# Kernel tuning notes

Measured on AMD Instinct MI355X. Metric: run time of the kernel, lower is better.

Reference implementation:

```python
import jax, jax.numpy as jnp
import numpy as np

B, S, D = 2, 2048, 2048
H, KVH, HD = 16, 4, 128
REP = H // KVH  # 4
THETA = 10000.0


def setup_inputs() -> dict:
    key = jax.random.key(0)
    ks = jax.random.split(key, 5)
    scale = 0.02
    x = jax.random.normal(ks[0], (B, S, D), dtype=jnp.float32)
    Wq = jax.random.normal(ks[1], (D, H * HD), dtype=jnp.float32) * scale
    Wk = jax.random.normal(ks[2], (D, KVH * HD), dtype=jnp.float32) * scale
    Wv = jax.random.normal(ks[3], (D, KVH * HD), dtype=jnp.float32) * scale
    Wo = jax.random.normal(ks[4], (H * HD, D), dtype=jnp.float32) * scale
    return {"x": x, "Wq": Wq, "Wk": Wk, "Wv": Wv, "Wo": Wo}


def _rope_cos_sin(seq_len, dtype):
    # HF-style rotary embedding: inv_freq over even dims, duplicated halves
    inv_freq = 1.0 / (THETA ** (jnp.arange(0, HD, 2, dtype=jnp.float32) / HD))
    pos = jnp.arange(seq_len, dtype=jnp.float32)
    ang = pos[:, None] * inv_freq[None, :]          # [S, HD/2]
    emb = jnp.concatenate([ang, ang], axis=-1)       # [S, HD]
    return jnp.cos(emb).astype(dtype), jnp.sin(emb).astype(dtype)


def _rotate_half(t):
    t1, t2 = jnp.split(t, 2, axis=-1)
    return jnp.concatenate([-t2, t1], axis=-1)


def reference(x, Wq, Wk, Wv, Wo):
    bsz, seq_len, _ = x.shape
    q = (x @ Wq).reshape(bsz, seq_len, H, HD).transpose(0, 2, 1, 3)    # [B,H,S,HD]
    k = (x @ Wk).reshape(bsz, seq_len, KVH, HD).transpose(0, 2, 1, 3)  # [B,KVH,S,HD]
    v = (x @ Wv).reshape(bsz, seq_len, KVH, HD).transpose(0, 2, 1, 3)
    cos, sin = _rope_cos_sin(seq_len, q.dtype)       # [S,HD]
    cos = cos[None, None, :, :]
    sin = sin[None, None, :, :]
    q = q * cos + _rotate_half(q) * sin
    k = k * cos + _rotate_half(k) * sin
    # repeat_interleave KV heads to match Q heads
    k = jnp.repeat(k, REP, axis=1)                   # [B,H,S,HD]
    v = jnp.repeat(v, REP, axis=1)
    scores = jnp.einsum('bhqd,bhkd->bhqk', q, k) / jnp.sqrt(jnp.float32(HD)).astype(q.dtype)
    i = jnp.arange(seq_len)
    causal = jnp.where(i[None, :] > i[:, None], jnp.float32(-jnp.inf), 0.0).astype(scores.dtype)
    scores = scores + causal[None, None, :, :]
    probs = jax.nn.softmax(scores.astype(jnp.float32), axis=-1).astype(q.dtype)
    out = jnp.einsum('bhqk,bhkd->bhqd', probs, v)    # [B,H,S,HD]
    out = out.transpose(0, 2, 1, 3).reshape(bsz, seq_len, H * HD)
    return out @ Wo
```

## Files before the change

### kernel.cpp

```cpp
#include <hip/hip_runtime.h>
#include <math.h>

#define B_   2
#define S_   2048
#define D_   2048
#define H_   16
#define KVH_ 4
#define HD_  128
#define REP_ 4

typedef __attribute__((ext_vector_type(8))) short bf16x8;
typedef __attribute__((ext_vector_type(4))) short bf16x4;
typedef __attribute__((ext_vector_type(4))) float f32x4;

#define QSCALE_LOG2E 0.1275266977097153f

__device__ __forceinline__ unsigned short f2bf(float x) {
    union { float f; unsigned u; } v; v.f = x;
    unsigned r = v.u + 0x7FFF + ((v.u >> 16) & 1);
    return (unsigned short)(r >> 16);
}

__device__ __forceinline__ unsigned short f2bf_fast(float x) {
    union { float f; unsigned u; } v; v.f = x;
    return (unsigned short)((v.u + 0x8000) >> 16);
}

__device__ __forceinline__ void gl_lds16(const unsigned short* g, unsigned short* l) {
    __builtin_amdgcn_global_load_lds(
        (const __attribute__((address_space(1))) unsigned int*)g,
        (__attribute__((address_space(3))) unsigned int*)l,
        16, 0, 0);
}

#define PH_BAR() do { asm volatile("" ::: "memory"); \
                      __builtin_amdgcn_s_barrier();  \
                      asm volatile("" ::: "memory"); } while (0)
#define VMW6 asm volatile("s_waitcnt vmcnt(6)" ::: "memory")
#define VMW4 asm volatile("s_waitcnt vmcnt(4)" ::: "memory")
#define VMW0 asm volatile("s_waitcnt vmcnt(0)" ::: "memory")

__global__ void cast_bf16(const float* __restrict__ src,
                          unsigned short* __restrict__ dst, int n4)
{
    int i = blockIdx.x * 256 + threadIdx.x;
    if (i >= n4) return;
    float4 v = *(const float4*)&src[(size_t)i * 4];
    bf16x4 o;
    o[0] = (short)f2bf(v.x); o[1] = (short)f2bf(v.y);
    o[2] = (short)f2bf(v.z); o[3] = (short)f2bf(v.w);
    *(bf16x4*)&dst[(size_t)i * 4] = o;
}

__global__ __launch_bounds__(256) void cast_transpose_all(
    const float* __restrict__ Wq, const float* __restrict__ Wk,
    const float* __restrict__ Wv, const float* __restrict__ Wo,
    unsigned short* __restrict__ Wqt, unsigned short* __restrict__ Wkt,
    unsigned short* __restrict__ Wvt, unsigned short* __restrict__ Wot)
{
    __shared__ float T[32][33];
    const int y = blockIdx.y;
    const float* src; unsigned short* dst; int C, bj;
    if (y < 64)      { src = Wq; dst = Wqt; C = 2048; bj = y; }
    else if (y < 80) { src = Wk; dst = Wkt; C = 512;  bj = y - 64; }
    else if (y < 96) { src = Wv; dst = Wvt; C = 512;  bj = y - 80; }
    else             { src = Wo; dst = Wot; C = 2048; bj = y - 96; }

    const int bi = blockIdx.x;
    const int t  = threadIdx.x;
    const int r  = t >> 3, cq = (t & 7) * 4;

    float4 v = *(const float4*)&src[(size_t)(bi * 32 + r) * C + bj * 32 + cq];
    T[r][cq + 0] = v.x; T[r][cq + 1] = v.y;
    T[r][cq + 2] = v.z; T[r][cq + 3] = v.w;
    __syncthreads();

    bf16x4 o;
    o[0] = (short)f2bf(T[cq + 0][r]);
    o[1] = (short)f2bf(T[cq + 1][r]);
    o[2] = (short)f2bf(T[cq + 2][r]);
    o[3] = (short)f2bf(T[cq + 3][r]);
    *(bf16x4*)&dst[(size_t)(bj * 32 + r) * 2048 + bi * 32 + cq] = o;
}

__global__ __launch_bounds__(512, 2) void qkv_mfma8(
    const unsigned short* __restrict__ Ah,
    const unsigned short* __restrict__ Wqt,
    const unsigned short* __restrict__ Wkt,
    const unsigned short* __restrict__ Wvt,
    unsigned short* __restrict__ Qh, unsigned short* __restrict__ Kh,
    unsigned short* __restrict__ Vt)
{
    __shared__ __align__(16) unsigned short lds[65536];

    const int bid = blockIdx.x;
    const int swz = (bid & 7) * 24 + (bid >> 3);
    const int bm = swz / 12, bn = swz % 12;
    const int m0 = bm * 256, n0 = bn * 256;

    const int tid  = threadIdx.x;
    const int w    = tid >> 6;
    const int lane = tid & 63;
    const int lo16 = lane & 15, quad = lane >> 4;
    const int wm   = w >> 2, wn = w & 3;

    const unsigned short* Bt;
    if (n0 < 2048)      Bt = Wqt + (size_t)n0 * 2048;
    else if (n0 < 2560) Bt = Wkt + (size_t)(n0 - 2048) * 2048;
    else                Bt = Wvt + (size_t)(n0 - 2560) * 2048;
    const unsigned short* Ag   = Ah + (size_t)m0 * 2048;
    const unsigned short* AgH1 = Ag + (size_t)128 * 2048;
    const unsigned short* BtH1 = Bt + (size_t)128 * 2048;

    const int rs   = lane >> 3;
    const int sce  = (((lane & 7) ^ rs) << 3);
    const int grow = w * 8 + rs;

    #define STAGE(gb, k0, lb) do {                                          \
        const unsigned short* _g = (gb) + (size_t)grow * 2048 + (k0) + sce; \
        gl_lds16(_g,                     (lb) + w * 512);                   \
        gl_lds16(_g + (size_t)64 * 2048, (lb) + (8 + w) * 512);             \
    } while (0)

    const int swb = (lo16 & 7) << 4;
    const int ac0 = (quad << 4) ^ swb;
    const int ac1 = (64 | (quad << 4)) ^ swb;
    char* ldsb = (char*)lds;
    const int abase = (wm * 128 + lo16) * 128;
    const int bbase = (wn * 16 + lo16) * 128 + 32768;

    f32x4 acc[8][4];
    #pragma unroll
    for (int mf = 0; mf < 8; ++mf)
        #pragma unroll
        for (int j = 0; j < 4; ++j) acc[mf][j] = (f32x4){0.f, 0.f, 0.f, 0.f};

    bf16x8 a0[4][2], a1[4][2], b0[2][2], b1[2][2];

    #define MM(Aa, Bb, mo, jo)                                               \
        _Pragma("unroll") for (int mf = 0; mf < 4; ++mf)                     \
        _Pragma("unroll") for (int j = 0; j < 2; ++j) {                      \
            acc[(mo)+mf][(jo)+j] = __builtin_amdgcn_mfma_f32_16x16x32_bf16(  \
                Aa[mf][0], Bb[j][0], acc[(mo)+mf][(jo)+j], 0, 0, 0);         \
            acc[(mo)+mf][(jo)+j] = __builtin_amdgcn_mfma_f32_16x16x32_bf16(  \
                Aa[mf][1], Bb[j][1], acc[(mo)+mf][(jo)+j], 0, 0, 0);         \
        }

    STAGE(Bt,   0,  lds + 16384);
    STAGE(BtH1, 0,  lds + 24576);
    STAGE(Ag,   0,  lds + 0);
    STAGE(AgH1, 0,  lds + 8192);
    STAGE(Bt,   64, lds + 32768 + 16384);
    STAGE(BtH1, 64, lds + 32768 + 24576);
    STAGE(Ag,   64, lds + 32768);
    VMW6;
    PH_BAR();

    #define PHASES(p, t)                                                         \
    {   _Pragma("unroll") for (int mf = 0; mf < 4; ++mf) {                       \
            a0[mf][0] = *(const bf16x8*)(ldsb + (p)*65536 + abase + mf*2048 + ac0); \
            a0[mf][1] = *(const bf16x8*)(ldsb + (p)*65536 + abase + mf*2048 + ac1); \
        }                                                                        \
        _Pragma("unroll") for (int j = 0; j < 2; ++j) {                          \
            b0[j][0] = *(const bf16x8*)(ldsb + (p)*65536 + bbase + j*8192 + ac0); \
            b0[j][1] = *(const bf16x8*)(ldsb + (p)*65536 + bbase + j*8192 + ac1); \
        }                                                                        \
        STAGE(AgH1, ((t)+1)*64, lds + ((p)^1)*32768 + 8192);                     \
        PH_BAR(); __builtin_amdgcn_s_setprio(1);                                 \
        MM(a0, b0, 0, 0);                                                        \
        __builtin_amdgcn_s_setprio(0); PH_BAR();                                 \
        _Pragma("unroll") for (int j = 0; j < 2; ++j) {                          \
            b1[j][0] = *(const bf16x8*)(ldsb + (p)*65536 + bbase + (j+2)*8192 + ac0); \
            b1[j][1] = *(const bf16x8*)(ldsb + (p)*65536 + bbase + (j+2)*8192 + ac1); \
        }                                                                        \
        STAGE(Bt, ((t)+2)*64, lds + (p)*32768 + 16384);                          \
        PH_BAR(); __builtin_amdgcn_s_setprio(1);                                 \
        MM(a0, b1, 0, 2);                                                        \
        __builtin_amdgcn_s_setprio(0); PH_BAR();                                 \
        _Pragma("unroll") for (int mf = 0; mf < 4; ++mf) {                       \
            a1[mf][0] = *(const bf16x8*)(ldsb + (p)*65536 + abase + (mf+4)*2048 + ac0); \
            a1[mf][1] = *(const bf16x8*)(ldsb + (p)*65536 + abase + (mf+4)*2048 + ac1); \
        }                                                                        \
        STAGE(BtH1, ((t)+2)*64, lds + (p)*32768 + 24576);                        \
        PH_BAR(); __builtin_amdgcn_s_setprio(1);                                 \
        MM(a1, b0, 4, 0);                                                        \
        __builtin_amdgcn_s_setprio(0); PH_BAR();                                 \
        STAGE(Ag, ((t)+2)*64, lds + (p)*32768);                                  \
        PH_BAR(); __builtin_amdgcn_s_setprio(1);                                 \
        MM(a1, b1, 4, 2);                                                        \
        __builtin_amdgcn_s_setprio(0);                                           \
        VMW6;                                                                    \
        PH_BAR();                                                                \
    }

    for (int it = 0; it < 16; ++it) {
        const int t = 2 * it;
        PHASES(0, t);
        PHASES(1, t + 1);
    }

    VMW0;
    PH_BAR();

    const int bb = m0 >> 11;
    const int s0loc = m0 & 2047;

    if (n0 < 2560) {
        const bool isQ = (n0 < 2048);
        const int h0 = isQ ? (n0 >> 7) : ((n0 - 2048) >> 7);
        const float post = isQ ? QSCALE_LOG2E : 1.0f;
        unsigned short* db[2];
        #pragma unroll
        for (int hp = 0; hp < 2; ++hp)
            db[hp] = isQ
                ? Qh + (((size_t)bb * H_   + h0 + hp) * S_) * HD_
                : Kh + (((size_t)bb * KVH_ + h0 + hp) * S_) * HD_;
        const int d = wn * 16 + lo16;
        const float inv = exp2f(-(float)d * 0.20761871093344086f);
        #pragma unroll
        for (int mf = 0; mf < 8; ++mf) {
            #pragma unroll
            for (int r = 0; r < 4; ++r) {
                int s = s0loc + wm * 128 + mf * 16 + quad * 4 + r;
                float sn, c;
                sincosf((float)s * inv, &sn, &c);
                #pragma unroll
                for (int hp = 0; hp < 2; ++hp) {
                    float lo = acc[mf][2 * hp + 0][r];
                    float hi = acc[mf][2 * hp + 1][r];
                    unsigned short* drow = db[hp] + (size_t)s * HD_;
                    drow[d]      = f2bf((lo * c - hi * sn) * post);
                    drow[d + 64] = f2bf((hi * c + lo * sn) * post);
                }
            }
        }
    } else {
        const int g0 = (n0 - 2560) >> 7;
        unsigned short* Ts = lds;
        const int d = wn * 16 + lo16;
        #pragma unroll
        for (int hp = 0; hp < 2; ++hp) {
            if (hp) PH_BAR();
            #pragma unroll
            for (int mf = 0; mf < 8; ++mf) {
                int ml = wm * 128 + mf * 16 + quad * 4;
                bf16x4 v0, v1;
                #pragma unroll
                for (int r = 0; r < 4; ++r) {
                    v0[r] = (short)f2bf(acc[mf][2 * hp + 0][r]);
                    v1[r] = (short)f2bf(acc[mf][2 * hp + 1][r]);
                }
                *(bf16x4*)&Ts[(size_t)d        * 264 + ml] = v0;
                *(bf16x4*)&Ts[(size_t)(d + 64) * 264 + ml] = v1;
            }
            PH_BAR();
            unsigned short* dstb = Vt + (((size_t)bb * KVH_ + g0 + hp) * HD_) * S_ + s0loc;
            #pragma unroll
            for (int itb = 0; itb < 8; ++itb) {
                int dd = itb * 16 + (tid >> 5);
                int ch = (tid & 31) * 8;
                *(bf16x8*)(dstb + (size_t)dd * S_ + ch) =
                    *(const bf16x8*)&Ts[(size_t)dd * 264 + ch];
            }
        }
    }
    #undef PHASES
    #undef MM
    #undef STAGE
}

__global__ __launch_bounds__(256, 2) void flash_attn_mfma(
    const unsigned short* __restrict__ Qh,
    const unsigned short* __restrict__ Kh,
    const unsigned short* __restrict__ Vt,
    unsigned short* __restrict__ attb)
{
    const int bh   = blockIdx.x;
    const int yy   = blockIdx.y;
    const int qt   = (yy < 8) ? (15 - yy) : (yy - 8);
    const int b    = bh >> 4, h = bh & 15;
    const int g    = h >> 2;
    const int tid  = threadIdx.x;
    const int w    = tid >> 6;
    const int lane = tid & 63;
    const int lo16 = lane & 15;
    const int quad = lane >> 4;

    const unsigned short* Qb = Qh + (((size_t)b * H_   + h) * S_) * HD_;
    const unsigned short* Kb = Kh + (((size_t)b * KVH_ + g) * S_) * HD_;
    const unsigned short* Vb = Vt + (((size_t)b * KVH_ + g) * HD_) * S_;

    __shared__ __align__(16) unsigned short Ks[64][136];
    __shared__ __align__(16) unsigned short Vs[128][72];
    __shared__ __align__(16) unsigned short Ps[4][32][72];

    const int q0 = qt * 128;
    const int qw = q0 + w * 32;

    bf16x8 qf[2][4];
    #pragma unroll
    for (int st = 0; st < 2; ++st)
        #pragma unroll
        for (int kc = 0; kc < 4; ++kc)
            qf[st][kc] = *(const bf16x8*)(Qb + (size_t)(qw + st * 16 + lo16) * HD_
                                             + kc * 32 + quad * 8);

    f32x4 o[2][8];
    #pragma unroll
    for (int st = 0; st < 2; ++st)
        #pragma unroll
        for (int n = 0; n < 8; ++n) o[st][n] = (f32x4){0.f, 0.f, 0.f, 0.f};
    float l_loc[2][4];
    #pragma unroll
    for (int st = 0; st < 2; ++st)
        #pragma unroll
        for (int r = 0; r < 4; ++r) l_loc[st][r] = 0.0f;

    const int kr = tid >> 4, kch = (tid & 15) * 8;
    const int vr = tid >> 3, vch = (tid & 7) * 8;

    bf16x8 kreg[4], vreg[4];
    #pragma unroll
    for (int i = 0; i < 4; ++i) {
        kreg[i] = *(const bf16x8*)(Kb + (size_t)(16 * i + kr) * HD_ + kch);
        vreg[i] = *(const bf16x8*)(Vb + (size_t)(32 * i + vr) * S_ + vch);
    }

    const int ktend = 2 * qt + 1;
    for (int kt = 0; kt <= ktend; ++kt) {
        const int k0 = kt * 64;
        __syncthreads();
        #pragma unroll
        for (int i = 0; i < 4; ++i) {
            *(bf16x8*)&Ks[16 * i + kr][kch] = kreg[i];
            *(bf16x8*)&Vs[32 * i + vr][vch] = vreg[i];
        }
        if (kt < ktend) {
            const int k0n = k0 + 64;
            #pragma unroll
            for (int i = 0; i < 4; ++i) {
                kreg[i] = *(const bf16x8*)(Kb + (size_t)(k0n + 16 * i + kr) * HD_ + kch);
                vreg[i] = *(const bf16x8*)(Vb + (size_t)(32 * i + vr) * S_ + k0n + vch);
            }
        }
        __syncthreads();

        if (w >= 2 || kt < ktend) {
            f32x4 sc[2][4];
            #pragma unroll
            for (int st = 0; st < 2; ++st)
                #pragma unroll
                for (int cb = 0; cb < 4; ++cb) sc[st][cb] = (f32x4){0.f, 0.f, 0.f, 0.f};
            #pragma unroll
            for (int kc = 0; kc < 4; ++kc)
                #pragma unroll
                for (int cb = 0; cb < 4; ++cb) {
                    bf16x8 kf = *(const bf16x8*)&Ks[cb * 16 + lo16][kc * 32 + quad * 8];
                    #pragma unroll
                    for (int st = 0; st < 2; ++st)
                        sc[st][cb] = __builtin_amdgcn_mfma_f32_16x16x32_bf16(
                            qf[st][kc], kf, sc[st][cb], 0, 0, 0);
                }

            const bool masked = (w < 2) ? (kt == 2 * qt) : (kt == ktend);
            if (masked) {
                #pragma unroll
                for (int st = 0; st < 2; ++st)
                    #pragma unroll
                    for (int r = 0; r < 4; ++r) {
                        const int row = qw + st * 16 + quad * 4 + r;
                        float lacc = 0.0f;
                        #pragma unroll
                        for (int cb = 0; cb < 4; ++cb) {
                            float xv = sc[st][cb][r];
                            if ((k0 + cb * 16 + lo16) > row) xv = -1e30f;
                            float p = exp2f(xv);
                            lacc += p;
                            Ps[w][st * 16 + quad * 4 + r][cb * 16 + lo16] = f2bf_fast(p);
                        }
                        l_loc[st][r] += lacc;
                    }
            } else {
                #pragma unroll
                for (int st = 0; st < 2; ++st)
                    #pragma unroll
                    for (int r = 0; r < 4; ++r) {
                        float lacc = 0.0f;
                        #pragma unroll
                        for (int cb = 0; cb < 4; ++cb) {
                            float p = exp2f(sc[st][cb][r]);
                            lacc += p;
                            Ps[w][st * 16 + quad * 4 + r][cb * 16 + lo16] = f2bf_fast(p);
                        }
                        l_loc[st][r] += lacc;
                    }
            }

            #pragma unroll
            for (int kc = 0; kc < 2; ++kc) {
                bf16x8 pf[2];
                #pragma unroll
                for (int st = 0; st < 2; ++st)
                    pf[st] = *(const bf16x8*)&Ps[w][st * 16 + lo16][kc * 32 + quad * 8];
                #pragma unroll
                for (int n = 0; n < 8; ++n) {
                    bf16x8 vf = *(const bf16x8*)&Vs[n * 16 + lo16][kc * 32 + quad * 8];
                    #pragma unroll
                    for (int st = 0; st < 2; ++st)
                        o[st][n] = __builtin_amdgcn_mfma_f32_16x16x32_bf16(
                            pf[st], vf, o[st][n], 0, 0, 0);
                }
            }
        }
    }

    #pragma unroll
    for (int st = 0; st < 2; ++st)
        #pragma unroll
        for (int r = 0; r < 4; ++r) {
            float l = l_loc[st][r];
            l += __shfl_xor(l, 1);
            l += __shfl_xor(l, 2);
            l += __shfl_xor(l, 4);
            l += __shfl_xor(l, 8);
            float invl = 1.0f / l;
            int srow = qw + st * 16 + quad * 4 + r;
            unsigned short* dst = attb + ((size_t)b * S_ + srow) * D_ + h * HD_;
            #pragma unroll
            for (int n = 0; n < 8; ++n)
                dst[n * 16 + lo16] = f2bf(o[st][n][r] * invl);
        }
}

__global__ __launch_bounds__(512, 2) void out_mfma8(
    const unsigned short* __restrict__ Ah,
    const unsigned short* __restrict__ Wot,
    float* __restrict__ C)
{
    __shared__ __align__(16) unsigned short lds[49152];

    const int bid = blockIdx.x;
    const int swz = (bid & 7) * 32 + (bid >> 3);
    const int bm = swz >> 4, bn = swz & 15;
    const int m0 = bm * 256, n0 = bn * 128;

    const int tid  = threadIdx.x;
    const int w    = tid >> 6;
    const int lane = tid & 63;
    const int lo16 = lane & 15, quad = lane >> 4;
    const int wm   = w >> 2, wn = w & 3;

    const unsigned short* Ag   = Ah  + (size_t)m0 * 2048;
    const unsigned short* AgH1 = Ag  + (size_t)128 * 2048;
    const unsigned short* Bt   = Wot + (size_t)n0 * 2048;

    const int rs   = lane >> 3;
    const int sce  = (((lane & 7) ^ rs) << 3);
    const int grow = w * 8 + rs;

    #define OSTAGE(gb, k0, lb) do {                                         \
        const unsigned short* _g = (gb) + (size_t)grow * 2048 + (k0) + sce; \
        gl_lds16(_g,                     (lb) + w * 512);                   \
        gl_lds16(_g + (size_t)64 * 2048, (lb) + (8 + w) * 512);             \
    } while (0)

    const int swb = (lo16 & 7) << 4;
    const int ac0 = (quad << 4) ^ swb;
    const int ac1 = (64 | (quad << 4)) ^ swb;
    char* ldsb = (char*)lds;
    const int abase = (wm * 128 + lo16) * 128;
    const int bbase = (wn * 32 + lo16) * 128 + 32768;

    f32x4 acc[8][2];
    #pragma unroll
    for (int mf = 0; mf < 8; ++mf)
        #pragma unroll
        for (int j = 0; j < 2; ++j) acc[mf][j] = (f32x4){0.f, 0.f, 0.f, 0.f};

    bf16x8 a0[4][2], a1[4][2], bb[2][2];

    #define OMM(Aa, mo, j)                                                   \
        _Pragma("unroll") for (int mf = 0; mf < 4; ++mf) {                   \
            acc[(mo)+mf][j] = __builtin_amdgcn_mfma_f32_16x16x32_bf16(       \
                Aa[mf][0], bb[j][0], acc[(mo)+mf][j], 0, 0, 0);              \
            acc[(mo)+mf][j] = __builtin_amdgcn_mfma_f32_16x16x32_bf16(       \
                Aa[mf][1], bb[j][1], acc[(mo)+mf][j], 0, 0, 0);              \
        }

    OSTAGE(Bt,   0,  lds + 16384);
    OSTAGE(Ag,   0,  lds + 0);
    OSTAGE(AgH1, 0,  lds + 8192);
    OSTAGE(Bt,   64, lds + 24576 + 16384);
    OSTAGE(Ag,   64, lds + 24576);
    VMW4;
    PH_BAR();

    #define OPH(p, t)                                                            \
    {             \
        _Pragma("unroll") for (int mf = 0; mf < 4; ++mf) {                       \
            a0[mf][0] = *(const bf16x8*)(ldsb + (p)*49152 + abase + mf*2048 + ac0); \
            a0[mf][1] = *(const bf16x8*)(ldsb + (p)*49152 + abase + mf*2048 + ac1); \
        }                                                                        \
        _Pragma("unroll") for (int j = 0; j < 2; ++j) {                          \
            bb[j][0] = *(const bf16x8*)(ldsb + (p)*49152 + bbase + j*2048 + ac0); \
            bb[j][1] = *(const bf16x8*)(ldsb + (p)*49152 + bbase + j*2048 + ac1); \
        }                                                                        \
        OSTAGE(AgH1, ((t)+1)*64, lds + ((p)^1)*24576 + 8192);                    \
        PH_BAR(); __builtin_amdgcn_s_setprio(1);                                 \
        OMM(a0, 0, 0);                                                           \
        __builtin_amdgcn_s_setprio(0); PH_BAR();                                 \
                                        \
        OSTAGE(Bt, ((t)+2)*64, lds + (p)*24576 + 16384);                         \
        PH_BAR(); __builtin_amdgcn_s_setprio(1);                                 \
        OMM(a0, 0, 1);                                                           \
        __builtin_amdgcn_s_setprio(0); PH_BAR();                                 \
                                                \
        _Pragma("unroll") for (int mf = 0; mf < 4; ++mf) {                       \
            a1[mf][0] = *(const bf16x8*)(ldsb + (p)*49152 + abase + (mf+4)*2048 + ac0); \
            a1[mf][1] = *(const bf16x8*)(ldsb + (p)*49152 + abase + (mf+4)*2048 + ac1); \
        }                                                                        \
        PH_BAR(); __builtin_amdgcn_s_setprio(1);                                 \
        OMM(a1, 4, 0);                                                           \
        __builtin_amdgcn_s_setprio(0); PH_BAR();                                 \
              \
        OSTAGE(Ag, ((t)+2)*64, lds + (p)*24576);                                 \
        PH_BAR(); __builtin_amdgcn_s_setprio(1);                                 \
        OMM(a1, 4, 1);                                                           \
        __builtin_amdgcn_s_setprio(0);                                           \
        VMW4;                                                                    \
        PH_BAR();                                                                \
    }

    for (int it = 0; it < 16; ++it) {
        const int t = 2 * it;
        OPH(0, t);
        OPH(1, t + 1);
    }

    VMW0;

    #pragma unroll
    for (int mf = 0; mf < 8; ++mf)
        #pragma unroll
        for (int r = 0; r < 4; ++r) {
            size_t m = (size_t)(m0 + wm * 128 + mf * 16 + quad * 4 + r);
            #pragma unroll
            for (int j = 0; j < 2; ++j)
                C[m * 2048 + n0 + wn * 32 + j * 16 + lo16] = acc[mf][j][r];
        }
    #undef OPH
    #undef OMM
    #undef OSTAGE
}

extern "C" void kernel_launch(void* const* d_in, const int* in_sizes, int n_in,
                              void* d_out, int out_size, void* d_ws, size_t ws_size,
                              hipStream_t stream)
{
    const float* x  = (const float*)d_in[0];
    const float* Wq = (const float*)d_in[1];
    const float* Wk = (const float*)d_in[2];
    const float* Wv = (const float*)d_in[3];
    const float* Wo = (const float*)d_in[4];
    float* out = (float*)d_out;

    unsigned short* xh  = (unsigned short*)d_ws;
    unsigned short* Wqt = xh  + (size_t)4096 * 2048;
    unsigned short* Wkt = Wqt + (size_t)2048 * 2048;
    unsigned short* Wvt = Wkt + (size_t)512 * 2048;
    unsigned short* Wot = Wvt + (size_t)512 * 2048;
    unsigned short* Qh  = Wot + (size_t)2048 * 2048;
    unsigned short* Kh  = Qh  + (size_t)B_ * H_   * S_ * HD_;
    unsigned short* Vt  = Kh  + (size_t)B_ * KVH_ * S_ * HD_;
    unsigned short* attb= xh;

    cast_bf16<<<(4096 * 2048 / 4 + 255) / 256, 256, 0, stream>>>(x, xh, 4096 * 2048 / 4);
    cast_transpose_all<<<dim3(64, 160), 256, 0, stream>>>(Wq, Wk, Wv, Wo, Wqt, Wkt, Wvt, Wot);

    qkv_mfma8<<<192, 512, 0, stream>>>(xh, Wqt, Wkt, Wvt, Qh, Kh, Vt);

    flash_attn_mfma<<<dim3(32, 16), 256, 0, stream>>>(Qh, Kh, Vt, attb);

    out_mfma8<<<256, 512, 0, stream>>>(attb, Wot, out);
}
```

Measured before the change: 279.6 us.

## Read K/V fragments directly from global memory and remap attention grid for L2 reuse

The flash attention kernel no longer stages K and V tiles through shared memory with block-wide barriers. Each wave now loads its MFMA K and V fragments straight from global memory and runs its own causal trip count. The 1D grid is also remapped so blocks that share a KV group and batch sit close in launch order, which should improve L2 hits on the shared K/V. This removes the LDS copies and __syncthreads, but each wave now issues many more global loads and depends on cache locality instead of explicit reuse.

```diff
diff --git a/kernel.cpp b/kernel.cpp
--- a/kernel.cpp
+++ b/kernel.cpp
@@ -275,11 +275,14 @@
     const unsigned short* __restrict__ Vt,
     unsigned short* __restrict__ attb)
 {
-    const int bh   = blockIdx.x;
-    const int yy   = blockIdx.y;
-    const int qt   = (yy < 8) ? (15 - yy) : (yy - 8);
-    const int b    = bh >> 4, h = bh & 15;
-    const int g    = h >> 2;
+    const int bid  = blockIdx.x;
+    const int b    = (bid >> 2) & 1;
+    const int g    = bid & 3;
+    const int j    = bid >> 3;
+    const int h    = g * 4 + (j & 3);
+    const int qidx = j >> 2;
+    const int qt   = (qidx < 8) ? (15 - qidx) : (qidx - 8);
+
     const int tid  = threadIdx.x;
     const int w    = tid >> 6;
     const int lane = tid & 63;
@@ -290,8 +293,6 @@
     const unsigned short* Kb = Kh + (((size_t)b * KVH_ + g) * S_) * HD_;
     const unsigned short* Vb = Vt + (((size_t)b * KVH_ + g) * HD_) * S_;
 
-    __shared__ __align__(16) unsigned short Ks[64][136];
-    __shared__ __align__(16) unsigned short Vs[128][72];
     __shared__ __align__(16) unsigned short Ps[4][32][72];
 
     const int q0 = qt * 128;
@@ -316,100 +317,75 @@
         #pragma unroll
         for (int r = 0; r < 4; ++r) l_loc[st][r] = 0.0f;
 
-    const int kr = tid >> 4, kch = (tid & 15) * 8;
-    const int vr = tid >> 3, vch = (tid & 7) * 8;
-
-    bf16x8 kreg[4], vreg[4];
-    #pragma unroll
-    for (int i = 0; i < 4; ++i) {
-        kreg[i] = *(const bf16x8*)(Kb + (size_t)(16 * i + kr) * HD_ + kch);
-        vreg[i] = *(const bf16x8*)(Vb + (size_t)(32 * i + vr) * S_ + vch);
-    }
-
-    const int ktend = 2 * qt + 1;
-    for (int kt = 0; kt <= ktend; ++kt) {
+    const int ktend_w = 2 * qt + (w >> 1);
+
+    for (int kt = 0; kt <= ktend_w; ++kt) {
         const int k0 = kt * 64;
-        __syncthreads();
-        #pragma unroll
-        for (int i = 0; i < 4; ++i) {
-            *(bf16x8*)&Ks[16 * i + kr][kch] = kreg[i];
-            *(bf16x8*)&Vs[32 * i + vr][vch] = vreg[i];
-        }
-        if (kt < ktend) {
-            const int k0n = k0 + 64;
-            #pragma unroll
-            for (int i = 0; i < 4; ++i) {
-                kreg[i] = *(const bf16x8*)(Kb + (size_t)(k0n + 16 * i + kr) * HD_ + kch);
-                vreg[i] = *(const bf16x8*)(Vb + (size_t)(32 * i + vr) * S_ + k0n + vch);
+
+        f32x4 sc[2][4];
+        #pragma unroll
+        for (int st = 0; st < 2; ++st)
+            #pragma unroll
+            for (int cb = 0; cb < 4; ++cb) sc[st][cb] = (f32x4){0.f, 0.f, 0.f, 0.f};
+        #pragma unroll
+        for (int kc = 0; kc < 4; ++kc)
+            #pragma unroll
+            for (int cb = 0; cb < 4; ++cb) {
+                bf16x8 kf = *(const bf16x8*)(Kb + (size_t)(k0 + cb * 16 + lo16) * HD_
+                                                + kc * 32 + quad * 8);
+                #pragma unroll
+                for (int st = 0; st < 2; ++st)
+                    sc[st][cb] = __builtin_amdgcn_mfma_f32_16x16x32_bf16(
+                        qf[st][kc], kf, sc[st][cb], 0, 0, 0);
             }
-        }
-        __syncthreads();
-
-        if (w >= 2 || kt < ktend) {
-            f32x4 sc[2][4];
+
+        if (kt == ktend_w) {
             #pragma unroll
             for (int st = 0; st < 2; ++st)
                 #pragma unroll
-                for (int cb = 0; cb < 4; ++cb) sc[st][cb] = (f32x4){0.f, 0.f, 0.f, 0.f};
-            #pragma unroll
-            for (int kc = 0; kc < 4; ++kc)
+                for (int r = 0; r < 4; ++r) {
+                    const int row = qw + st * 16 + quad * 4 + r;
+                    float lacc = 0.0f;
+                    #pragma unroll
+                    for (int cb = 0; cb < 4; ++cb) {
+                        float xv = sc[st][cb][r];
+                        if ((k0 + cb * 16 + lo16) > row) xv = -1e30f;
+                        float p = exp2f(xv);
+                        lacc += p;
+                        Ps[w][st * 16 + quad * 4 + r][cb * 16 + lo16] = f2bf_fast(p);
+                    }
+                    l_loc[st][r] += lacc;
+                }
+        } else {
+            #pragma unroll
+            for (int st = 0; st < 2; ++st)
                 #pragma unroll
-                for (int cb = 0; cb < 4; ++cb) {
-                    bf16x8 kf = *(const bf16x8*)&Ks[cb * 16 + lo16][kc * 32 + quad * 8];
+                for (int r = 0; r < 4; ++r) {
+                    float lacc = 0.0f;
                     #pragma unroll
-                    for (int st = 0; st < 2; ++st)
-                        sc[st][cb] = __builtin_amdgcn_mfma_f32_16x16x32_bf16(
-                            qf[st][kc], kf, sc[st][cb], 0, 0, 0);
+                    for (int cb = 0; cb < 4; ++cb) {
+                        float p = exp2f(sc[st][cb][r]);
+                        lacc += p;
+                        Ps[w][st * 16 + quad * 4 + r][cb * 16 + lo16] = f2bf_fast(p);
+                    }
+                    l_loc[st][r] += lacc;
                 }
-
-            const bool masked = (w < 2) ? (kt == 2 * qt) : (kt == ktend);
-            if (masked) {
+        }
+
+        #pragma unroll
+        for (int kc = 0; kc < 2; ++kc) {
+            bf16x8 pf[2];
+            #pragma unroll
+            for (int st = 0; st < 2; ++st)
+                pf[st] = *(const bf16x8*)&Ps[w][st * 16 + lo16][kc * 32 + quad * 8];
+            #pragma unroll
+            for (int n = 0; n < 8; ++n) {
+                bf16x8 vf = *(const bf16x8*)(Vb + (size_t)(n * 16 + lo16) * S_
+                                                + k0 + kc * 32 + quad * 8);
                 #pragma unroll
                 for (int st = 0; st < 2; ++st)
-                    #pragma unroll
-                    for (int r = 0; r < 4; ++r) {
-                        const int row = qw + st * 16 + quad * 4 + r;
-                        float lacc = 0.0f;
-                        #pragma unroll
-                        for (int cb = 0; cb < 4; ++cb) {
-                            float xv = sc[st][cb][r];
-                            if ((k0 + cb * 16 + lo16) > row) xv = -1e30f;
-                            float p = exp2f(xv);
-                            lacc += p;
-                            Ps[w][st * 16 + quad * 4 + r][cb * 16 + lo16] = f2bf_fast(p);
-                        }
-                        l_loc[st][r] += lacc;
-                    }
-            } else {
-                #pragma unroll
-                for (int st = 0; st < 2; ++st)
-                    #pragma unroll
-                    for (int r = 0; r < 4; ++r) {
-                        float lacc = 0.0f;
-                        #pragma unroll
-                        for (int cb = 0; cb < 4; ++cb) {
-                            float p = exp2f(sc[st][cb][r]);
-                            lacc += p;
-                            Ps[w][st * 16 + quad * 4 + r][cb * 16 + lo16] = f2bf_fast(p);
-                        }
-                        l_loc[st][r] += lacc;
-                    }
-            }
-
-            #pragma unroll
-            for (int kc = 0; kc < 2; ++kc) {
-                bf16x8 pf[2];
-                #pragma unroll
-                for (int st = 0; st < 2; ++st)
-                    pf[st] = *(const bf16x8*)&Ps[w][st * 16 + lo16][kc * 32 + quad * 8];
-                #pragma unroll
-                for (int n = 0; n < 8; ++n) {
-                    bf16x8 vf = *(const bf16x8*)&Vs[n * 16 + lo16][kc * 32 + quad * 8];
-                    #pragma unroll
-                    for (int st = 0; st < 2; ++st)
-                        o[st][n] = __builtin_amdgcn_mfma_f32_16x16x32_bf16(
-                            pf[st], vf, o[st][n], 0, 0, 0);
-                }
+                    o[st][n] = __builtin_amdgcn_mfma_f32_16x16x32_bf16(
+                        pf[st], vf, o[st][n], 0, 0, 0);
             }
         }
     }
@@ -496,8 +472,7 @@
     PH_BAR();
 
     #define OPH(p, t)                                                            \
-    {             \
-        _Pragma("unroll") for (int mf = 0; mf < 4; ++mf) {                       \
+    {   _Pragma("unroll") for (int mf = 0; mf < 4; ++mf) {                       \
             a0[mf][0] = *(const bf16x8*)(ldsb + (p)*49152 + abase + mf*2048 + ac0); \
             a0[mf][1] = *(const bf16x8*)(ldsb + (p)*49152 + abase + mf*2048 + ac1); \
         }                                                                        \
@@ -509,12 +484,10 @@
         PH_BAR(); __builtin_amdgcn_s_setprio(1);                                 \
         OMM(a0, 0, 0);                                                           \
         __builtin_amdgcn_s_setprio(0); PH_BAR();                                 \
-                                        \
         OSTAGE(Bt, ((t)+2)*64, lds + (p)*24576 + 16384);                         \
         PH_BAR(); __builtin_amdgcn_s_setprio(1);                                 \
         OMM(a0, 0, 1);                                                           \
         __builtin_amdgcn_s_setprio(0); PH_BAR();                                 \
-                                                \
         _Pragma("unroll") for (int mf = 0; mf < 4; ++mf) {                       \
             a1[mf][0] = *(const bf16x8*)(ldsb + (p)*49152 + abase + (mf+4)*2048 + ac0); \
             a1[mf][1] = *(const bf16x8*)(ldsb + (p)*49152 + abase + (mf+4)*2048 + ac1); \
@@ -522,7 +495,6 @@
         PH_BAR(); __builtin_amdgcn_s_setprio(1);                                 \
         OMM(a1, 4, 0);                                                           \
         __builtin_amdgcn_s_setprio(0); PH_BAR();                                 \
-              \
         OSTAGE(Ag, ((t)+2)*64, lds + (p)*24576);                                 \
         PH_BAR(); __builtin_amdgcn_s_setprio(1);                                 \
         OMM(a1, 4, 1);                                                           \
@@ -579,7 +551,7 @@
 
     qkv_mfma8<<<192, 512, 0, stream>>>(xh, Wqt, Wkt, Wvt, Qh, Kh, Vt);
 
-    flash_attn_mfma<<<dim3(32, 16), 256, 0, stream>>>(Qh, Kh, Vt, attb);
+    flash_attn_mfma<<<512, 256, 0, stream>>>(Qh, Kh, Vt, attb);
 
     out_mfma8<<<256, 512, 0, stream>>>(attb, Wot, out);
 }
```

Result: slower. 355.9 us (+27.3%).
